# Kernel optimization log

Measured on AMD Instinct MI355X. Metric: run time of the kernel, lower is better.

## Reference

```python
import jax, jax.numpy as jnp
import numpy as np

N_NODES = 50000
N_EDGES = 640000
D_IN = 128
HIDDEN = 128
OUT = 64


def sage_conv(x, edge_index, W_l, b_l, W_r):
    # PyG SAGEConv (mean aggr): out = lin_l(mean_j x_j) + lin_r(x_i)
    src, dst = edge_index[0], edge_index[1]
    msgs = x[src]                                             # [E, d] gather
    agg = jax.ops.segment_sum(msgs, dst, num_segments=x.shape[0])
    cnt = jax.ops.segment_sum(jnp.ones((edge_index.shape[1],), x.dtype), dst,
                              num_segments=x.shape[0])
    mean = agg / jnp.maximum(cnt, 1.0)[:, None]
    return mean @ W_l.T + b_l + x @ W_r.T


def setup_inputs() -> dict:
    key = jax.random.key(0)
    ks = jax.random.split(key, 8)
    s = lambda d: 1.0 / np.sqrt(d)
    x = jax.random.normal(ks[0], (N_NODES, D_IN), dtype=jnp.float32)
    edge_index = jax.random.randint(ks[1], (2, N_EDGES), 0, N_NODES, dtype=jnp.int64)
    return {
        "x": x,
        "edge_index": edge_index,
        "W1_l": jax.random.normal(ks[2], (HIDDEN, D_IN), jnp.float32) * s(D_IN),
        "b1_l": jnp.zeros((HIDDEN,), jnp.float32),
        "W1_r": jax.random.normal(ks[3], (HIDDEN, D_IN), jnp.float32) * s(D_IN),
        "W2_l": jax.random.normal(ks[4], (HIDDEN, HIDDEN), jnp.float32) * s(HIDDEN),
        "b2_l": jnp.zeros((HIDDEN,), jnp.float32),
        "W2_r": jax.random.normal(ks[5], (HIDDEN, HIDDEN), jnp.float32) * s(HIDDEN),
        "W3": jax.random.normal(ks[6], (OUT, HIDDEN), jnp.float32) * s(HIDDEN),
        "b3": jnp.zeros((OUT,), jnp.float32),
    }


def reference(x, edge_index, W1_l, b1_l, W1_r, W2_l, b2_l, W2_r, W3, b3):
    h = jax.nn.relu(sage_conv(x, edge_index, W1_l, b1_l, W1_r))
    h = jax.nn.relu(sage_conv(h, edge_index, W2_l, b2_l, W2_r))
    return h @ W3.T + b3
```

## Files before the change

kernel.cpp:

```cpp
#include <hip/hip_runtime.h>
#include <hip/hip_fp16.h>


typedef _Float16 f16x8 __attribute__((ext_vector_type(8)));
typedef float floatx4 __attribute__((ext_vector_type(4)));
typedef float floatx2 __attribute__((ext_vector_type(2)));

__device__ __forceinline__ unsigned short f2h(float f) {
    __half h = __float2half_rn(f);
    union { __half h; unsigned short s; } c; c.h = h; return c.s;
}
__device__ __forceinline__ __half2 u2h(unsigned u) {
    union { unsigned u; __half2 h; } c; c.u = u; return c.h;
}
__device__ __forceinline__ unsigned h2u(__half2 h) {
    union { __half2 h; unsigned u; } c; c.h = h; return c.u;
}
__device__ __forceinline__ __half2 shx(__half2 v, int m) {
    return u2h((unsigned)__shfl_xor((int)h2u(v), m, 64));
}
__device__ __forceinline__ ushort4 cvt4h(float4 v) {
    ushort4 o;
    o.x = f2h(v.x); o.y = f2h(v.y); o.z = f2h(v.z); o.w = f2h(v.w);
    return o;
}
__device__ __forceinline__ unsigned char f2fp8(float v) {
    return (unsigned char)(__builtin_amdgcn_cvt_pk_fp8_f32(v, v, 0, false) & 0xff);
}

#define WSEG 18432
__global__ __launch_bounds__(256) void prologue_kernel(
    const float* __restrict__ W1l, const float* __restrict__ W1r,
    const float* __restrict__ W2l, const float* __restrict__ W2r,
    const float* __restrict__ W3,  const float* __restrict__ x,
    unsigned short* __restrict__ wb,
    unsigned short* __restrict__ xb,
    unsigned char* __restrict__ x8,
    int* __restrict__ deg, int NX4, int ND4)
{
    int i = blockIdx.x * 256 + threadIdx.x;
    if (i < WSEG) {
        const float* s; int l;
        if (i < 8192)       { if (i < 4096) { s = W1l; l = i; }
                              else          { s = W1r; l = i - 4096; } }
        else if (i < 16384) { if (i < 12288){ s = W2l; l = i - 8192; }
                              else          { s = W2r; l = i - 12288; } }
        else                { s = W3; l = i - 16384; }
        ((ushort4*)wb)[i] = cvt4h(((const float4*)s)[l]);
        return;
    }
    int j = i - WSEG;
    if (j < NX4) {
        float4 v = ((const float4*)x)[j];
        ((ushort4*)xb)[j] = cvt4h(v);
        unsigned u8 = __builtin_amdgcn_cvt_pk_fp8_f32(v.x, v.y, 0, false);
        u8 = __builtin_amdgcn_cvt_pk_fp8_f32(v.z, v.w, u8, true);
        ((unsigned*)x8)[j] = u8;
        return;
    }
    int k = j - NX4;
    if (k < ND4) ((int4*)deg)[k] = make_int4(0, 0, 0, 0);
}

__global__ __launch_bounds__(256) void hist_kernel(const int* __restrict__ dst,
                                                   int* __restrict__ deg, int E) {
    int e = blockIdx.x * 256 + threadIdx.x;
    if (e < E) atomicAdd(deg + dst[e], 1);
}

__global__ __launch_bounds__(256) void scan_partial_kernel(
    const int* __restrict__ deg, int* __restrict__ partials, int N)
{
    __shared__ int ws[4];
    const int t = threadIdx.x, lane = t & 63, wave = t >> 6;
    const int i4 = blockIdx.x * 256 + t;
    const int n4 = (N + 3) / 4;
    int s = 0;
    if (i4 < n4) {
        int b = i4 * 4;
        if (b + 3 < N) {
            int4 v = ((const int4*)deg)[i4];
            s = v.x + v.y + v.z + v.w;
        } else {
            for (int q = 0; q < 4 && b + q < N; ++q) s += deg[b + q];
        }
    }
#pragma unroll
    for (int off = 32; off > 0; off >>= 1) s += __shfl_xor(s, off, 64);
    if (lane == 0) ws[wave] = s;
    __syncthreads();
    if (t == 0) partials[blockIdx.x] = ws[0] + ws[1] + ws[2] + ws[3];
}

__global__ __launch_bounds__(256) void scan_apply_kernel(
    const int* __restrict__ deg, const int* __restrict__ partials,
    int* __restrict__ rowptr, int* __restrict__ cursor, int N, int P)
{
    __shared__ int woff[4];
    __shared__ int s_base;
    const int t = threadIdx.x, lane = t & 63, wave = t >> 6;
    const int i4 = blockIdx.x * 256 + t;
    const int n4 = (N + 3) / 4;
    const int b = i4 * 4;

    if (wave == 0) {
        int v = (lane < P && lane < (int)blockIdx.x) ? partials[lane] : 0;
#pragma unroll
        for (int off = 32; off > 0; off >>= 1) v += __shfl_xor(v, off, 64);
        if (lane == 0) s_base = v;
    }

    int4 v = make_int4(0, 0, 0, 0);
    if (i4 < n4) {
        if (b + 3 < N) v = ((const int4*)deg)[i4];
        else {
            if (b + 0 < N) v.x = deg[b + 0];
            if (b + 1 < N) v.y = deg[b + 1];
            if (b + 2 < N) v.z = deg[b + 2];
        }
    }
    const int p1 = v.x, p2 = v.x + v.y, p3 = v.x + v.y + v.z;
    const int tsum = p3 + v.w;
    int incl = tsum;
#pragma unroll
    for (int off = 1; off < 64; off <<= 1) {
        int tt = __shfl_up(incl, off, 64);
        if (lane >= off) incl += tt;
    }
    const int texcl = incl - tsum;
    if (lane == 63) woff[wave] = incl;
    __syncthreads();
    int wo = 0;
#pragma unroll
    for (int w = 0; w < 4; ++w) if (w < wave) wo += woff[w];
    const int e = s_base + wo + texcl;
    if (blockIdx.x == 0 && t == 0) rowptr[0] = 0;
    if (b + 3 < N) {
        ((int4*)cursor)[i4] = make_int4(e, e + p1, e + p2, e + p3);
        rowptr[b + 1] = e + p1;
        rowptr[b + 2] = e + p2;
        rowptr[b + 3] = e + p3;
        rowptr[b + 4] = e + tsum;
    } else if (b < N) {
        if (b + 0 < N) { cursor[b + 0] = e;      rowptr[b + 1] = e + p1; }
        if (b + 1 < N) { cursor[b + 1] = e + p1; rowptr[b + 2] = e + p2; }
        if (b + 2 < N) { cursor[b + 2] = e + p2; rowptr[b + 3] = e + p3; }
    }
}

__global__ __launch_bounds__(256) void fill_kernel(const int* __restrict__ src,
                                                   const int* __restrict__ dst,
                                                   int* __restrict__ cursor,
                                                   int* __restrict__ csr, int E) {
    int e = blockIdx.x * 256 + threadIdx.x;
    if (e >= E) return;
    int pos = atomicAdd(cursor + dst[e], 1);
    csr[pos] = src[e];
}

template <bool WFP8, bool HEAD>
__global__ __launch_bounds__(256) void sage_layer_kernel(
    const unsigned short* __restrict__ feat,
    const unsigned char* __restrict__ feat8,
    const int* __restrict__ rowptr, const int* __restrict__ csr,
    const unsigned short* __restrict__ Wl,
    const unsigned short* __restrict__ Wr,
    const float* __restrict__ bias,
    unsigned short* __restrict__ out,
    unsigned char* __restrict__ out8,
    const unsigned short* __restrict__ W3,
    const float* __restrict__ b3,
    float* __restrict__ outF,
    int N)
{
    __shared__ unsigned short smean[16][136];
    __shared__ unsigned short sh2[HEAD ? 16 : 1][136];
    const int wave = threadIdx.x >> 6;
    const int lane = threadIdx.x & 63;
    const int r0 = blockIdx.x * 16;

    {
        const int grp = lane >> 4;
        const int col = lane & 15;
        const unsigned char* fq = feat8 + col * 8;

        int w[5];
#pragma unroll
        for (int q = 0; q < 5; ++q) {
            int n = r0 + wave * 4 + q;
            w[q] = rowptr[n < N ? n : N];
        }

        auto consume = [&](int mi, int beg, int end, uint2 pay[4]) {
            const int deg = end - beg;
            floatx2 a0 = (floatx2)(0.f), a1 = (floatx2)(0.f);
            floatx2 a2 = (floatx2)(0.f), a3 = (floatx2)(0.f);
#pragma unroll
            for (int c = 0; c < 4; ++c) {
                const int j = beg + grp + c * 4;
                const unsigned m = (j < end) ? 0xffffffffu : 0u;
                uint2 p = pay[c];
                p.x &= m; p.y &= m;
                a0 += __builtin_amdgcn_cvt_pk_f32_fp8(p.x, false);
                a1 += __builtin_amdgcn_cvt_pk_f32_fp8(p.x, true);
                a2 += __builtin_amdgcn_cvt_pk_f32_fp8(p.y, false);
                a3 += __builtin_amdgcn_cvt_pk_f32_fp8(p.y, true);
            }
            for (int jA = beg + 16 + grp; jA < end; jA += 16) {
                const int jB = jA + 4, jC = jA + 8, jD = jA + 12;
                const unsigned mB = (jB < end) ? 0xffffffffu : 0u;
                const unsigned mC = (jC < end) ? 0xffffffffu : 0u;
                const unsigned mD = (jD < end) ? 0xffffffffu : 0u;
                const int iA = csr[jA];
                const int iB = csr[mB ? jB : beg];
                const int iC = csr[mC ? jC : beg];
                const int iD = csr[mD ? jD : beg];
                uint2 pA = *(const uint2*)(fq + (size_t)iA * 128);
                uint2 pB = *(const uint2*)(fq + (size_t)iB * 128);
                uint2 pC = *(const uint2*)(fq + (size_t)iC * 128);
                uint2 pD = *(const uint2*)(fq + (size_t)iD * 128);
                pB.x &= mB; pB.y &= mB;
                pC.x &= mC; pC.y &= mC;
                pD.x &= mD; pD.y &= mD;
                a0 += __builtin_amdgcn_cvt_pk_f32_fp8(pA.x, false);
                a1 += __builtin_amdgcn_cvt_pk_f32_fp8(pA.x, true);
                a2 += __builtin_amdgcn_cvt_pk_f32_fp8(pA.y, false);
                a3 += __builtin_amdgcn_cvt_pk_f32_fp8(pA.y, true);
                a0 += __builtin_amdgcn_cvt_pk_f32_fp8(pB.x, false);
                a1 += __builtin_amdgcn_cvt_pk_f32_fp8(pB.x, true);
                a2 += __builtin_amdgcn_cvt_pk_f32_fp8(pB.y, false);
                a3 += __builtin_amdgcn_cvt_pk_f32_fp8(pB.y, true);
                a0 += __builtin_amdgcn_cvt_pk_f32_fp8(pC.x, false);
                a1 += __builtin_amdgcn_cvt_pk_f32_fp8(pC.x, true);
                a2 += __builtin_amdgcn_cvt_pk_f32_fp8(pC.y, false);
                a3 += __builtin_amdgcn_cvt_pk_f32_fp8(pC.y, true);
                a0 += __builtin_amdgcn_cvt_pk_f32_fp8(pD.x, false);
                a1 += __builtin_amdgcn_cvt_pk_f32_fp8(pD.x, true);
                a2 += __builtin_amdgcn_cvt_pk_f32_fp8(pD.y, false);
                a3 += __builtin_amdgcn_cvt_pk_f32_fp8(pD.y, true);
            }
            __half2 c0 = __floats2half2_rn(a0.x, a0.y);
            __half2 c1 = __floats2half2_rn(a1.x, a1.y);
            __half2 c2 = __floats2half2_rn(a2.x, a2.y);
            __half2 c3 = __floats2half2_rn(a3.x, a3.y);
            c0 = __hadd2(c0, shx(c0, 16)); c0 = __hadd2(c0, shx(c0, 32));
            c1 = __hadd2(c1, shx(c1, 16)); c1 = __hadd2(c1, shx(c1, 32));
            c2 = __hadd2(c2, shx(c2, 16)); c2 = __hadd2(c2, shx(c2, 32));
            c3 = __hadd2(c3, shx(c3, 16)); c3 = __hadd2(c3, shx(c3, 32));
            if (grp == 0) {
                const float inv = (deg > 0) ? 1.0f / (float)deg : 0.0f;
                uint4 o;
                o.x = h2u(__floats2half2_rn(__low2float(c0) * inv,
                                            __high2float(c0) * inv));
                o.y = h2u(__floats2half2_rn(__low2float(c1) * inv,
                                            __high2float(c1) * inv));
                o.z = h2u(__floats2half2_rn(__low2float(c2) * inv,
                                            __high2float(c2) * inv));
                o.w = h2u(__floats2half2_rn(__low2float(c3) * inv,
                                            __high2float(c3) * inv));
                *(uint4*)&smean[mi][col * 8] = o;
            }
        };

#pragma unroll
        for (int p = 0; p < 2; ++p) {
            const int qa = 2 * p, qb = 2 * p + 1;
            const int begA = w[qa], endA = w[qa + 1];
            const int begB = w[qb], endB = w[qb + 1];
            int idxA[4], idxB[4];
#pragma unroll
            for (int c = 0; c < 4; ++c) {
                const int j = begA + grp + c * 4;
                idxA[c] = csr[j < endA ? j : 0];
            }
#pragma unroll
            for (int c = 0; c < 4; ++c) {
                const int j = begB + grp + c * 4;
                idxB[c] = csr[j < endB ? j : 0];
            }
            uint2 payA[4], payB[4];
#pragma unroll
            for (int c = 0; c < 4; ++c)
                payA[c] = *(const uint2*)(fq + (size_t)idxA[c] * 128);
#pragma unroll
            for (int c = 0; c < 4; ++c)
                payB[c] = *(const uint2*)(fq + (size_t)idxB[c] * 128);
            consume(wave * 4 + qa, begA, endA, payA);
            consume(wave * 4 + qb, begB, endB, payB);
        }
    }
    __syncthreads();

    const int mrow = lane & 15;
    const int quad = lane >> 4;
    int selfRow = r0 + mrow;
    if (selfRow >= N) selfRow = N - 1;
    const size_t rowS = (size_t)selfRow * 128;

    floatx4 acc0 = (floatx4)(0.0f), acc1 = (floatx4)(0.0f);
    const int t0 = wave * 2, t1 = wave * 2 + 1;

#pragma unroll
    for (int kk = 0; kk < 4; ++kk) {
        const int k = kk * 32 + quad * 8;
        f16x8 aA = *(const f16x8*)&smean[mrow][k];
        f16x8 aS = *(const f16x8*)(feat + rowS + k);
        f16x8 bl0 = *(const f16x8*)(Wl + (size_t)(t0 * 16 + mrow) * 128 + k);
        acc0 = __builtin_amdgcn_mfma_f32_16x16x32_f16(aA, bl0, acc0, 0, 0, 0);
        f16x8 br0 = *(const f16x8*)(Wr + (size_t)(t0 * 16 + mrow) * 128 + k);
        acc0 = __builtin_amdgcn_mfma_f32_16x16x32_f16(aS, br0, acc0, 0, 0, 0);
        f16x8 bl1 = *(const f16x8*)(Wl + (size_t)(t1 * 16 + mrow) * 128 + k);
        acc1 = __builtin_amdgcn_mfma_f32_16x16x32_f16(aA, bl1, acc1, 0, 0, 0);
        f16x8 br1 = *(const f16x8*)(Wr + (size_t)(t1 * 16 + mrow) * 128 + k);
        acc1 = __builtin_amdgcn_mfma_f32_16x16x32_f16(aS, br1, acc1, 0, 0, 0);
    }

    const float b0 = bias[t0 * 16 + mrow];
    const float b1 = bias[t1 * 16 + mrow];
#pragma unroll
    for (int i = 0; i < 4; ++i) {
        const int r = r0 + quad * 4 + i;
        const float v0 = fmaxf(acc0[i] + b0, 0.0f);
        const float v1 = fmaxf(acc1[i] + b1, 0.0f);
        if (HEAD) {
            sh2[quad * 4 + i][t0 * 16 + mrow] = f2h(v0);
            sh2[quad * 4 + i][t1 * 16 + mrow] = f2h(v1);
        } else if (r < N) {
            out[(size_t)r * 128 + t0 * 16 + mrow] = f2h(v0);
            out[(size_t)r * 128 + t1 * 16 + mrow] = f2h(v1);
            if (WFP8) {
                out8[(size_t)r * 128 + t0 * 16 + mrow] = f2fp8(v0);
                out8[(size_t)r * 128 + t1 * 16 + mrow] = f2fp8(v1);
            }
        }
    }

    if (HEAD) {
        __syncthreads();
        floatx4 ah = (floatx4)(0.0f);
#pragma unroll
        for (int kk = 0; kk < 4; ++kk) {
            const int k = kk * 32 + quad * 8;
            f16x8 aA = *(const f16x8*)&sh2[mrow][k];
            f16x8 b = *(const f16x8*)(W3 + (size_t)(wave * 16 + mrow) * 128 + k);
            ah = __builtin_amdgcn_mfma_f32_16x16x32_f16(aA, b, ah, 0, 0, 0);
        }
        const float bh = b3[wave * 16 + mrow];
#pragma unroll
        for (int i = 0; i < 4; ++i) {
            const int r = r0 + quad * 4 + i;
            if (r < N)
                outF[(size_t)r * 64 + wave * 16 + mrow] = ah[i] + bh;
        }
    }
}

extern "C" void kernel_launch(void* const* d_in, const int* in_sizes, int n_in,
                              void* d_out, int out_size, void* d_ws, size_t ws_size,
                              hipStream_t stream)
{
    const float* x   = (const float*)d_in[0];
    const int* ei    = (const int*)d_in[1];
    const float* W1l = (const float*)d_in[2];
    const float* b1l = (const float*)d_in[3];
    const float* W1r = (const float*)d_in[4];
    const float* W2l = (const float*)d_in[5];
    const float* b2l = (const float*)d_in[6];
    const float* W2r = (const float*)d_in[7];
    const float* W3  = (const float*)d_in[8];
    const float* b3  = (const float*)d_in[9];
    float* out = (float*)d_out;

    const int N = in_sizes[0] / 128;
    const int E = in_sizes[1] / 2;
    const int* src = ei;
    const int* dst = ei + E;

    const int n4 = (N + 3) / 4;
    int* deg_i    = (int*)d_ws;
    int* partials = deg_i + n4 * 4;
    int* rowptr   = partials + 64;
    int* cursor   = rowptr + N + 4;
    int* csr      = cursor + n4 * 4;
    unsigned short* xb   = (unsigned short*)(csr + E);
    unsigned short* h1   = xb + (size_t)N * 128;
    unsigned short* wb1l = h1 + (size_t)N * 128;
    unsigned short* wb1r = wb1l + 16384;
    unsigned short* wb2l = wb1r + 16384;
    unsigned short* wb2r = wb2l + 16384;
    unsigned short* wb3  = wb2r + 16384;
    unsigned char* x8    = (unsigned char*)(wb3 + 8192);
    unsigned char* h18   = x8 + (size_t)N * 128;

    const int lblk = (N + 15) / 16;
    const int eblk = (E + 255) / 256;
    const int NX4  = N * 32;
    const int P    = (n4 + 255) / 256;

    {
        int total = WSEG + NX4 + n4;
        hipLaunchKernelGGL(prologue_kernel, dim3((total + 255) / 256), dim3(256), 0,
                           stream, W1l, W1r, W2l, W2r, W3, x, wb1l, xb, x8, deg_i,
                           NX4, n4);
    }

    hipLaunchKernelGGL(hist_kernel, dim3(eblk), dim3(256), 0, stream, dst, deg_i, E);
    hipLaunchKernelGGL(scan_partial_kernel, dim3(P), dim3(256), 0, stream,
                       deg_i, partials, N);
    hipLaunchKernelGGL(scan_apply_kernel, dim3(P), dim3(256), 0, stream,
                       deg_i, partials, rowptr, cursor, N, P);
    hipLaunchKernelGGL(fill_kernel, dim3(eblk), dim3(256), 0, stream,
                       src, dst, cursor, csr, E);

    hipLaunchKernelGGL((sage_layer_kernel<true, false>), dim3(lblk), dim3(256), 0,
                       stream, xb, x8, rowptr, csr, wb1l, wb1r, b1l,
                       h1, h18, nullptr, nullptr, nullptr, N);
    hipLaunchKernelGGL((sage_layer_kernel<false, true>), dim3(lblk), dim3(256), 0,
                       stream, h1, h18, rowptr, csr, wb2l, wb2r, b2l,
                       nullptr, nullptr, wb3, b3, out, N);
}
```

Before: 259.1 us.

## Fuse conversion with degree histogram and collapse scan into single-block kernel

Merges the weight/feature conversion and degree histogram into one grid-stride kernel, and replaces the two-pass scan with a single 1024-thread block that scans sequentially with a carry. The degree array is now zeroed with a memset, and the histogram and CSR fill read destination and source indices as int4, four edges per thread. The goal is fewer kernel launches and less per-edge overhead in the graph-preprocessing stage. The trade-off is a serial single-block scan over about 12.5k int4 chunks, and the fused kernel runs conversion and atomics in sequence within each thread.

```diff
diff --git a/kernel.cpp b/kernel.cpp
--- a/kernel.cpp
+++ b/kernel.cpp
@@ -29,122 +29,99 @@
 }
 
 #define WSEG 18432
-__global__ __launch_bounds__(256) void prologue_kernel(
+__global__ __launch_bounds__(256) void cvt_hist_kernel(
     const float* __restrict__ W1l, const float* __restrict__ W1r,
     const float* __restrict__ W2l, const float* __restrict__ W2r,
     const float* __restrict__ W3,  const float* __restrict__ x,
     unsigned short* __restrict__ wb,
     unsigned short* __restrict__ xb,
     unsigned char* __restrict__ x8,
-    int* __restrict__ deg, int NX4, int ND4)
+    const int* __restrict__ dst,
+    int* __restrict__ deg,
+    int NX4, int E)
 {
-    int i = blockIdx.x * 256 + threadIdx.x;
-    if (i < WSEG) {
-        const float* s; int l;
-        if (i < 8192)       { if (i < 4096) { s = W1l; l = i; }
-                              else          { s = W1r; l = i - 4096; } }
-        else if (i < 16384) { if (i < 12288){ s = W2l; l = i - 8192; }
-                              else          { s = W2r; l = i - 12288; } }
-        else                { s = W3; l = i - 16384; }
-        ((ushort4*)wb)[i] = cvt4h(((const float4*)s)[l]);
-        return;
-    }
-    int j = i - WSEG;
-    if (j < NX4) {
+    const int gsz  = gridDim.x * 256;
+    const int gtid = blockIdx.x * 256 + threadIdx.x;
+    const int total0 = WSEG + NX4;
+
+    for (int i = gtid; i < total0; i += gsz) {
+        if (i < WSEG) {
+            const float* s; int l;
+            if (i < 8192)       { if (i < 4096) { s = W1l; l = i; }
+                                  else          { s = W1r; l = i - 4096; } }
+            else if (i < 16384) { if (i < 12288){ s = W2l; l = i - 8192; }
+                                  else          { s = W2r; l = i - 12288; } }
+            else                { s = W3; l = i - 16384; }
+            ((ushort4*)wb)[i] = cvt4h(((const float4*)s)[l]);
+            continue;
+        }
+        int j = i - WSEG;
         float4 v = ((const float4*)x)[j];
         ((ushort4*)xb)[j] = cvt4h(v);
         unsigned u8 = __builtin_amdgcn_cvt_pk_fp8_f32(v.x, v.y, 0, false);
         u8 = __builtin_amdgcn_cvt_pk_fp8_f32(v.z, v.w, u8, true);
         ((unsigned*)x8)[j] = u8;
-        return;
-    }
-    int k = j - NX4;
-    if (k < ND4) ((int4*)deg)[k] = make_int4(0, 0, 0, 0);
-}
-
-__global__ __launch_bounds__(256) void hist_kernel(const int* __restrict__ dst,
-                                                   int* __restrict__ deg, int E) {
-    int e = blockIdx.x * 256 + threadIdx.x;
-    if (e < E) atomicAdd(deg + dst[e], 1);
-}
-
-__global__ __launch_bounds__(256) void scan_partial_kernel(
-    const int* __restrict__ deg, int* __restrict__ partials, int N)
+    }
+
+    const int E4 = E >> 2;
+    for (int i = gtid; i < E4; i += gsz) {
+        int4 d = ((const int4*)dst)[i];
+        atomicAdd(deg + d.x, 1);
+        atomicAdd(deg + d.y, 1);
+        atomicAdd(deg + d.z, 1);
+        atomicAdd(deg + d.w, 1);
+    }
+    for (int e = (E4 << 2) + gtid; e < E; e += gsz)
+        atomicAdd(deg + dst[e], 1);
+}
+
+__global__ __launch_bounds__(1024) void scan_kernel(
+    const int* __restrict__ deg, int* __restrict__ rowptr,
+    int* __restrict__ cursor, int N)
 {
-    __shared__ int ws[4];
+    __shared__ int wsum[16];
+    __shared__ int carry_s;
     const int t = threadIdx.x, lane = t & 63, wave = t >> 6;
-    const int i4 = blockIdx.x * 256 + t;
     const int n4 = (N + 3) / 4;
-    int s = 0;
-    if (i4 < n4) {
-        int b = i4 * 4;
-        if (b + 3 < N) {
-            int4 v = ((const int4*)deg)[i4];
-            s = v.x + v.y + v.z + v.w;
-        } else {
-            for (int q = 0; q < 4 && b + q < N; ++q) s += deg[b + q];
-        }
-    }
-#pragma unroll
-    for (int off = 32; off > 0; off >>= 1) s += __shfl_xor(s, off, 64);
-    if (lane == 0) ws[wave] = s;
+
+    if (t == 0) { carry_s = 0; rowptr[0] = 0; }
     __syncthreads();
-    if (t == 0) partials[blockIdx.x] = ws[0] + ws[1] + ws[2] + ws[3];
-}
-
-__global__ __launch_bounds__(256) void scan_apply_kernel(
-    const int* __restrict__ deg, const int* __restrict__ partials,
-    int* __restrict__ rowptr, int* __restrict__ cursor, int N, int P)
-{
-    __shared__ int woff[4];
-    __shared__ int s_base;
-    const int t = threadIdx.x, lane = t & 63, wave = t >> 6;
-    const int i4 = blockIdx.x * 256 + t;
-    const int n4 = (N + 3) / 4;
-    const int b = i4 * 4;
-
-    if (wave == 0) {
-        int v = (lane < P && lane < (int)blockIdx.x) ? partials[lane] : 0;
-#pragma unroll
-        for (int off = 32; off > 0; off >>= 1) v += __shfl_xor(v, off, 64);
-        if (lane == 0) s_base = v;
-    }
-
-    int4 v = make_int4(0, 0, 0, 0);
-    if (i4 < n4) {
-        if (b + 3 < N) v = ((const int4*)deg)[i4];
-        else {
-            if (b + 0 < N) v.x = deg[b + 0];
-            if (b + 1 < N) v.y = deg[b + 1];
-            if (b + 2 < N) v.z = deg[b + 2];
-        }
-    }
-    const int p1 = v.x, p2 = v.x + v.y, p3 = v.x + v.y + v.z;
-    const int tsum = p3 + v.w;
-    int incl = tsum;
-#pragma unroll
-    for (int off = 1; off < 64; off <<= 1) {
-        int tt = __shfl_up(incl, off, 64);
-        if (lane >= off) incl += tt;
-    }
-    const int texcl = incl - tsum;
-    if (lane == 63) woff[wave] = incl;
-    __syncthreads();
-    int wo = 0;
-#pragma unroll
-    for (int w = 0; w < 4; ++w) if (w < wave) wo += woff[w];
-    const int e = s_base + wo + texcl;
-    if (blockIdx.x == 0 && t == 0) rowptr[0] = 0;
-    if (b + 3 < N) {
-        ((int4*)cursor)[i4] = make_int4(e, e + p1, e + p2, e + p3);
-        rowptr[b + 1] = e + p1;
-        rowptr[b + 2] = e + p2;
-        rowptr[b + 3] = e + p3;
-        rowptr[b + 4] = e + tsum;
-    } else if (b < N) {
-        if (b + 0 < N) { cursor[b + 0] = e;      rowptr[b + 1] = e + p1; }
-        if (b + 1 < N) { cursor[b + 1] = e + p1; rowptr[b + 2] = e + p2; }
-        if (b + 2 < N) { cursor[b + 2] = e + p2; rowptr[b + 3] = e + p3; }
+
+    for (int base = 0; base < n4; base += 1024) {
+        const int i4 = base + t;
+        int4 v = make_int4(0, 0, 0, 0);
+        if (i4 < n4) v = ((const int4*)deg)[i4];
+        const int p1 = v.x, p2 = v.x + v.y, p3 = v.x + v.y + v.z;
+        const int tsum = p3 + v.w;
+
+        int incl = tsum;
+#pragma unroll
+        for (int off = 1; off < 64; off <<= 1) {
+            int tt = __shfl_up(incl, off, 64);
+            if (lane >= off) incl += tt;
+        }
+        if (lane == 63) wsum[wave] = incl;
+        __syncthreads();
+
+        int wo = 0;
+        for (int w = 0; w < 16; ++w) if (w < wave) wo += wsum[w];
+        const int e = carry_s + wo + (incl - tsum);
+
+        if (i4 < n4) {
+            const int b = i4 * 4;
+            ((int4*)cursor)[i4] = make_int4(e, e + p1, e + p2, e + p3);
+            rowptr[b + 1] = e + p1;
+            rowptr[b + 2] = e + p2;
+            rowptr[b + 3] = e + p3;
+            rowptr[b + 4] = e + tsum;
+        }
+        __syncthreads();
+        if (t == 0) {
+            int tot = 0;
+            for (int w = 0; w < 16; ++w) tot += wsum[w];
+            carry_s += tot;
+        }
+        __syncthreads();
     }
 }
 
@@ -152,10 +129,21 @@
                                                    const int* __restrict__ dst,
                                                    int* __restrict__ cursor,
                                                    int* __restrict__ csr, int E) {
-    int e = blockIdx.x * 256 + threadIdx.x;
-    if (e >= E) return;
-    int pos = atomicAdd(cursor + dst[e], 1);
-    csr[pos] = src[e];
+    const int E4 = E >> 2;
+    int i = blockIdx.x * 256 + threadIdx.x;
+    if (i < E4) {
+        int4 d = ((const int4*)dst)[i];
+        int4 s = ((const int4*)src)[i];
+        int p0 = atomicAdd(cursor + d.x, 1); csr[p0] = s.x;
+        int p1 = atomicAdd(cursor + d.y, 1); csr[p1] = s.y;
+        int p2 = atomicAdd(cursor + d.z, 1); csr[p2] = s.z;
+        int p3 = atomicAdd(cursor + d.w, 1); csr[p3] = s.w;
+    }
+    int e = (E4 << 2) + i;
+    if (i < (E - (E4 << 2))) {
+        int pos = atomicAdd(cursor + dst[e], 1);
+        csr[pos] = src[e];
+    }
 }
 
 template <bool WFP8, bool HEAD>
@@ -393,23 +381,19 @@
     unsigned char* h18   = x8 + (size_t)N * 128;
 
     const int lblk = (N + 15) / 16;
-    const int eblk = (E + 255) / 256;
     const int NX4  = N * 32;
-    const int P    = (n4 + 255) / 256;
-
-    {
-        int total = WSEG + NX4 + n4;
-        hipLaunchKernelGGL(prologue_kernel, dim3((total + 255) / 256), dim3(256), 0,
-                           stream, W1l, W1r, W2l, W2r, W3, x, wb1l, xb, x8, deg_i,
-                           NX4, n4);
-    }
-
-    hipLaunchKernelGGL(hist_kernel, dim3(eblk), dim3(256), 0, stream, dst, deg_i, E);
-    hipLaunchKernelGGL(scan_partial_kernel, dim3(P), dim3(256), 0, stream,
-                       deg_i, partials, N);
-    hipLaunchKernelGGL(scan_apply_kernel, dim3(P), dim3(256), 0, stream,
-                       deg_i, partials, rowptr, cursor, N, P);
-    hipLaunchKernelGGL(fill_kernel, dim3(eblk), dim3(256), 0, stream,
+    const int E4   = E >> 2;
+
+    hipMemsetAsync(deg_i, 0, (size_t)n4 * 16, stream);
+
+    hipLaunchKernelGGL(cvt_hist_kernel, dim3(2048), dim3(256), 0, stream,
+                       W1l, W1r, W2l, W2r, W3, x, wb1l, xb, x8, dst, deg_i,
+                       NX4, E);
+
+    hipLaunchKernelGGL(scan_kernel, dim3(1), dim3(1024), 0, stream,
+                       deg_i, rowptr, cursor, N);
+
+    hipLaunchKernelGGL(fill_kernel, dim3((E4 + 255) / 256), dim3(256), 0, stream,
                        src, dst, cursor, csr, E);
 
     hipLaunchKernelGGL((sage_layer_kernel<true, false>), dim3(lblk), dim3(256), 0,
```

Result: slower. 270.6 us (+4.4%).
